# Kernel optimization log

Hardware: AMD Instinct MI355X
Metric: run time of the kernel (lower is better)

Reference implementation:

```python
import jax, jax.numpy as jnp
import numpy as np

NUM_USERS = 200000
NUM_ITEMS = 100000
N = NUM_USERS + NUM_ITEMS
EMB_DIM = 64
NUM_LAYERS = 3
NNZ = 4000000


def setup_inputs() -> dict:
    key = jax.random.key(0)
    k1, k2, k3, k4, k5 = jax.random.split(key, 5)
    # xavier_uniform: bound = sqrt(6/(fan_in+fan_out))
    bound = float(np.sqrt(6.0 / (NUM_USERS + EMB_DIM)))
    user_emb = jax.random.uniform(k1, (NUM_USERS, EMB_DIM), jnp.float32, -bound, bound)
    bound_i = float(np.sqrt(6.0 / (NUM_ITEMS + EMB_DIM)))
    item_emb = jax.random.uniform(k2, (NUM_ITEMS, EMB_DIM), jnp.float32, -bound_i, bound_i)
    rows = jax.random.randint(k3, (NNZ,), 0, N, dtype=jnp.int32)
    cols = jax.random.randint(k4, (NNZ,), 0, N, dtype=jnp.int32)
    vals = jax.random.uniform(k5, (NNZ,), jnp.float32)
    return {"user_emb": user_emb, "item_emb": item_emb,
            "rows": rows, "cols": cols, "vals": vals}


def _spmm(rows, cols, vals, x):
    # sparse (N,N) @ dense (N,D) via gather + segment-sum scatter
    gathered = vals[:, None] * x[cols]          # [nnz, D]
    return jax.ops.segment_sum(gathered, rows, num_segments=N)


def reference(user_emb, item_emb, rows, cols, vals):
    emb = jnp.concatenate([user_emb, item_emb], axis=0)  # [N, D]
    acc = emb  # running sum fuses the layer-mean (avoids stacking all layers)
    for _ in range(NUM_LAYERS):
        emb = _spmm(rows, cols, vals, emb)
        acc = acc + emb
    final = acc / (NUM_LAYERS + 1)
    return final[:NUM_USERS], final[NUM_USERS:]
```

## Files before the change

kernel.cpp:

```cpp
#include <hip/hip_runtime.h>


#define NUSERS 200000
#define NITEMS 100000
#define NNODES 300000
#define DIM 64
#define NNZ_CNT 4000000

#define SCAN_CHUNK 1024
#define NCHUNKS ((NNODES + SCAN_CHUNK - 1) / SCAN_CHUNK)
#define CNT_PAD (NCHUNKS * SCAN_CHUNK)

#define BSHIFT 10
#define BROWS  (1 << BSHIFT)
#define NB     ((NNODES + BROWS - 1) >> BSHIFT)
#define EPB    8192


__device__ __forceinline__ unsigned short f32_to_bf16(float f) {
    unsigned u = __float_as_uint(f);
    u += 0x7FFFu + ((u >> 16) & 1u);
    return (unsigned short)(u >> 16);
}
__device__ __forceinline__ float bf16_to_f32(unsigned short h) {
    return __uint_as_float(((unsigned)h) << 16);
}


__global__ void k_hist(const int* __restrict__ rows, int* __restrict__ cnt) {
    int e = blockIdx.x * blockDim.x + threadIdx.x;
    if (e >= NNZ_CNT) return;
    atomicAdd(&cnt[rows[e]], 1);
}

__global__ void k_partial(const int* __restrict__ cnt, int* __restrict__ partial) {
    int t = threadIdx.x;
    int base = blockIdx.x * SCAN_CHUNK;
    int4 c = ((const int4*)(cnt + base))[t];
    int tsum = c.x + c.y + c.z + c.w;
    __shared__ int lds[256];
    lds[t] = tsum; __syncthreads();
    for (int d = 128; d > 0; d >>= 1) {
        if (t < d) lds[t] += lds[t + d];
        __syncthreads();
    }
    if (t == 0) partial[blockIdx.x] = lds[0];
}

__global__ void k_scanpartial(const int* __restrict__ partial, int* __restrict__ partoff) {
    int t = threadIdx.x;
    int v = (t < NCHUNKS) ? partial[t] : 0;
    __shared__ int lds[512];
    lds[t] = v; __syncthreads();
    for (int d = 1; d < 512; d <<= 1) {
        int cur = lds[t];
        int add = (t >= d) ? lds[t - d] : 0;
        __syncthreads();
        lds[t] = cur + add;
        __syncthreads();
    }
    if (t < NCHUNKS) partoff[t] = lds[t] - v;
}

__global__ void k_scan3(const int* __restrict__ cnt, const int* __restrict__ partoff,
                        int* __restrict__ rowptr) {
    int t = threadIdx.x, b = blockIdx.x;
    int base = b * SCAN_CHUNK;
    int4 c = ((const int4*)(cnt + base))[t];
    int tsum = c.x + c.y + c.z + c.w;
    __shared__ int lds[256];
    lds[t] = tsum; __syncthreads();
    for (int d = 1; d < 256; d <<= 1) {
        int cur = lds[t];
        int add = (t >= d) ? lds[t - d] : 0;
        __syncthreads();
        lds[t] = cur + add;
        __syncthreads();
    }
    int excl = lds[t] - tsum;
    int off = partoff[b] + excl;
    int idx = base + t * 4;
    rowptr[idx + 0] = off;
    rowptr[idx + 1] = off + c.x;
    rowptr[idx + 2] = off + c.x + c.y;
    rowptr[idx + 3] = off + c.x + c.y + c.z;
}

__global__ void k_initcur(const int* __restrict__ rowptr, int* __restrict__ gcursor) {
    int t = blockIdx.x * blockDim.x + threadIdx.x;
    if (t >= NB) return;
    int r = t << BSHIFT;
    if (r > NNODES) r = NNODES;
    gcursor[t] = rowptr[r];
}


__global__ void __launch_bounds__(256) k_bucketA(
        const int* __restrict__ rows, const int* __restrict__ cols,
        const float* __restrict__ vals, int* __restrict__ gcursor,
        int2* __restrict__ staged) {
    __shared__ int hist[NB];
    __shared__ int lbase[NB];
    __shared__ int lcur[NB];
    int t = threadIdx.x;
    int e0 = blockIdx.x * EPB;
    for (int i = t; i < NB; i += 256) { hist[i] = 0; lcur[i] = 0; }
    __syncthreads();
    for (int k = 0; k < EPB / 256; ++k) {
        int e = e0 + k * 256 + t;
        if (e < NNZ_CNT) atomicAdd(&hist[rows[e] >> BSHIFT], 1);
    }
    __syncthreads();
    for (int i = t; i < NB; i += 256) {
        int h = hist[i];
        lbase[i] = h ? atomicAdd(&gcursor[i], h) : 0;
    }
    __syncthreads();
    for (int k = 0; k < EPB / 256; ++k) {
        int e = e0 + k * 256 + t;
        if (e >= NNZ_CNT) continue;
        int r = rows[e];
        int b = r >> BSHIFT;
        int p = lbase[b] + atomicAdd(&lcur[b], 1);
        int2 rec;
        rec.x = ((r & (BROWS - 1)) << 19) | cols[e];
        rec.y = __float_as_int(vals[e]);
        staged[p] = rec;
    }
}


__global__ void __launch_bounds__(1024) k_bucketB(
        const int* __restrict__ rowptr, const int2* __restrict__ staged,
        int2* __restrict__ packed) {
    __shared__ int cur[BROWS];
    int b = blockIdx.x;
    int t = threadIdx.x;
    int r0 = b << BSHIFT;
    int r1 = min(r0 + BROWS, NNODES);
    int nrows = r1 - r0;
    for (int i = t; i < nrows; i += 1024) cur[i] = rowptr[r0 + i];
    __syncthreads();
    int start = rowptr[r0];
    int end   = rowptr[r1];
    for (int idx = start + t; idx < end; idx += 1024) {
        int2 rec = staged[idx];
        int rel = ((unsigned)rec.x) >> 19;
        int col = rec.x & 0x7FFFF;
        int pos = atomicAdd(&cur[rel], 1);
        int2 out; out.x = col; out.y = rec.y;
        packed[pos] = out;
    }
}


__global__ void k_init0(const float* __restrict__ ue, const float* __restrict__ ie,
                        unsigned short* __restrict__ xb0, float* __restrict__ acc) {
    int i = blockIdx.x * blockDim.x + threadIdx.x;
    const int total = NNODES * DIM / 4;
    if (i >= total) return;
    const int userEnd = NUSERS * DIM / 4;
    float4 v = (i < userEnd) ? ((const float4*)ue)[i]
                             : ((const float4*)ie)[i - userEnd];
    ((float4*)acc)[i] = v;
    ushort4 h;
    h.x = f32_to_bf16(v.x); h.y = f32_to_bf16(v.y);
    h.z = f32_to_bf16(v.z); h.w = f32_to_bf16(v.w);
    ((ushort4*)xb0)[i] = h;
}


template <int FINAL>
__global__ void __launch_bounds__(256) k_spmm_csr(
                           const int* __restrict__ rowptr, const int2* __restrict__ packed,
                           const unsigned short* __restrict__ xin,
                           unsigned short* __restrict__ y, float* __restrict__ acc) {
    int row  = blockIdx.x * (blockDim.x >> 6) + (threadIdx.x >> 6);
    int lane = threadIdx.x & 63;
    if (row >= NNODES) return;
    int start = __builtin_amdgcn_readfirstlane(rowptr[row]);
    int end   = __builtin_amdgcn_readfirstlane(rowptr[row + 1]);
    const unsigned short* __restrict__ xl = xin + lane;
    float s0 = 0.f, s1 = 0.f, s2 = 0.f, s3 = 0.f;
    int idx = start;
    for (; idx + 4 <= end; idx += 4) {
        int2 e0 = packed[idx + 0];
        int2 e1 = packed[idx + 1];
        int2 e2 = packed[idx + 2];
        int2 e3 = packed[idx + 3];
        float g0 = bf16_to_f32(xl[(size_t)e0.x << 6]);
        float g1 = bf16_to_f32(xl[(size_t)e1.x << 6]);
        float g2 = bf16_to_f32(xl[(size_t)e2.x << 6]);
        float g3 = bf16_to_f32(xl[(size_t)e3.x << 6]);
        s0 += __int_as_float(e0.y) * g0;
        s1 += __int_as_float(e1.y) * g1;
        s2 += __int_as_float(e2.y) * g2;
        s3 += __int_as_float(e3.y) * g3;
    }
    for (; idx < end; ++idx) {
        int2 e = packed[idx];
        s0 += __int_as_float(e.y) * bf16_to_f32(xl[(size_t)e.x << 6]);
    }
    float s = (s0 + s1) + (s2 + s3);
    size_t o = ((size_t)row << 6) + lane;
    if (FINAL) {
        acc[o] = (acc[o] + s) * 0.25f;
    } else {
        y[o] = f32_to_bf16(s);
        acc[o] += s;
    }
}


extern "C" void kernel_launch(void* const* d_in, const int* in_sizes, int n_in,
                              void* d_out, int out_size, void* d_ws, size_t ws_size,
                              hipStream_t stream) {
    const float* ue   = (const float*)d_in[0];
    const float* ie   = (const float*)d_in[1];
    const int*   rows = (const int*)d_in[2];
    const int*   cols = (const int*)d_in[3];
    const float* vals = (const float*)d_in[4];
    float* acc = (float*)d_out;

    const size_t embN = (size_t)NNODES * DIM;
    char* p = (char*)d_ws;
    unsigned short* xb0 = (unsigned short*)p;  p += embN * 2;
    unsigned short* xb1 = (unsigned short*)p;  p += embN * 2;
    unsigned short* xb2 = (unsigned short*)p;  p += embN * 2;
    int*   rowptr = (int*)p;              p += (size_t)(CNT_PAD + 16) * 4;
    int*   cnt    = (int*)p;              p += (size_t)(CNT_PAD + 16) * 4;
    int*   part   = (int*)p;              p += 512 * 4;
    int*   poff   = (int*)p;              p += 512 * 4;
    int*   gcur   = (int*)p;              p += 512 * 4;
    int2*  staged = (int2*)p;             p += (size_t)NNZ_CNT * 8;
    int2*  packed = (int2*)p;             p += (size_t)NNZ_CNT * 8;

    const int edge_blocks = (NNZ_CNT + 255) / 256;
    const int row_blocks  = (NNODES + 3) / 4;
    const int bucketA_blocks = (NNZ_CNT + EPB - 1) / EPB;
    const int vec_blocks = (NNODES * DIM / 4 + 255) / 256;

    hipMemsetAsync(cnt, 0, (size_t)(CNT_PAD + 16) * 4, stream);
    k_hist<<<edge_blocks, 256, 0, stream>>>(rows, cnt);
    k_partial<<<NCHUNKS, 256, 0, stream>>>(cnt, part);
    k_scanpartial<<<1, 512, 0, stream>>>(part, poff);
    k_scan3<<<NCHUNKS, 256, 0, stream>>>(cnt, poff, rowptr);

    k_initcur<<<2, 256, 0, stream>>>(rowptr, gcur);
    k_bucketA<<<bucketA_blocks, 256, 0, stream>>>(rows, cols, vals, gcur, staged);
    k_bucketB<<<NB, 1024, 0, stream>>>(rowptr, staged, packed);

    k_init0<<<vec_blocks, 256, 0, stream>>>(ue, ie, xb0, acc);

    k_spmm_csr<0><<<row_blocks, 256, 0, stream>>>(rowptr, packed, xb0, xb1, acc);
    k_spmm_csr<0><<<row_blocks, 256, 0, stream>>>(rowptr, packed, xb1, xb2, acc);
    k_spmm_csr<1><<<row_blocks, 256, 0, stream>>>(rowptr, packed, xb2, (unsigned short*)nullptr, acc);
}
```

Measured before the change: 869.3 us.

## Build CSR via bucket-level histogram and in-block row scan; prefetch SpMM edges

Replaces the per-row global atomic histogram and three-kernel scan with a per-bucket histogram that uses shared-memory atomics, a single-block bucket scan, and a per-bucket row count and scan inside k_bucketB that writes rowptr directly. This removes 4M contended global atomics and several small kernel launches from the CSR build. The SpMM kernel also switches to an 8-wide loop that software-prefetches the next 8 packed edges, with masked tail handling, to hide edge-load latency behind the gathers. The costs are an extra pass over staged records in bucketB, and padded edge loads and gathers for short rows.

```diff
diff --git a/kernel.cpp b/kernel.cpp
--- a/kernel.cpp
+++ b/kernel.cpp
@@ -7,10 +7,6 @@
 #define DIM 64
 #define NNZ_CNT 4000000
 
-#define SCAN_CHUNK 1024
-#define NCHUNKS ((NNODES + SCAN_CHUNK - 1) / SCAN_CHUNK)
-#define CNT_PAD (NCHUNKS * SCAN_CHUNK)
-
 #define BSHIFT 10
 #define BROWS  (1 << BSHIFT)
 #define NB     ((NNODES + BROWS - 1) >> BSHIFT)
@@ -27,29 +23,28 @@
 }
 
 
-__global__ void k_hist(const int* __restrict__ rows, int* __restrict__ cnt) {
-    int e = blockIdx.x * blockDim.x + threadIdx.x;
-    if (e >= NNZ_CNT) return;
-    atomicAdd(&cnt[rows[e]], 1);
-}
-
-__global__ void k_partial(const int* __restrict__ cnt, int* __restrict__ partial) {
-    int t = threadIdx.x;
-    int base = blockIdx.x * SCAN_CHUNK;
-    int4 c = ((const int4*)(cnt + base))[t];
-    int tsum = c.x + c.y + c.z + c.w;
-    __shared__ int lds[256];
-    lds[t] = tsum; __syncthreads();
-    for (int d = 128; d > 0; d >>= 1) {
-        if (t < d) lds[t] += lds[t + d];
-        __syncthreads();
-    }
-    if (t == 0) partial[blockIdx.x] = lds[0];
-}
-
-__global__ void k_scanpartial(const int* __restrict__ partial, int* __restrict__ partoff) {
-    int t = threadIdx.x;
-    int v = (t < NCHUNKS) ? partial[t] : 0;
+__global__ void __launch_bounds__(256) k_bhist(const int* __restrict__ rows,
+                                               int* __restrict__ bcnt) {
+    __shared__ int hist[NB];
+    int t = threadIdx.x;
+    int e0 = blockIdx.x * EPB;
+    for (int i = t; i < NB; i += 256) hist[i] = 0;
+    __syncthreads();
+    for (int k = 0; k < EPB / 256; ++k) {
+        int e = e0 + k * 256 + t;
+        if (e < NNZ_CNT) atomicAdd(&hist[rows[e] >> BSHIFT], 1);
+    }
+    __syncthreads();
+    for (int i = t; i < NB; i += 256) {
+        int h = hist[i];
+        if (h) atomicAdd(&bcnt[i], h);
+    }
+}
+
+__global__ void k_bscan(const int* __restrict__ bcnt, int* __restrict__ bbase,
+                        int* __restrict__ gcur) {
+    int t = threadIdx.x;
+    int v = (t < NB) ? bcnt[t] : 0;
     __shared__ int lds[512];
     lds[t] = v; __syncthreads();
     for (int d = 1; d < 512; d <<= 1) {
@@ -59,39 +54,12 @@
         lds[t] = cur + add;
         __syncthreads();
     }
-    if (t < NCHUNKS) partoff[t] = lds[t] - v;
-}
-
-__global__ void k_scan3(const int* __restrict__ cnt, const int* __restrict__ partoff,
-                        int* __restrict__ rowptr) {
-    int t = threadIdx.x, b = blockIdx.x;
-    int base = b * SCAN_CHUNK;
-    int4 c = ((const int4*)(cnt + base))[t];
-    int tsum = c.x + c.y + c.z + c.w;
-    __shared__ int lds[256];
-    lds[t] = tsum; __syncthreads();
-    for (int d = 1; d < 256; d <<= 1) {
-        int cur = lds[t];
-        int add = (t >= d) ? lds[t - d] : 0;
-        __syncthreads();
-        lds[t] = cur + add;
-        __syncthreads();
-    }
-    int excl = lds[t] - tsum;
-    int off = partoff[b] + excl;
-    int idx = base + t * 4;
-    rowptr[idx + 0] = off;
-    rowptr[idx + 1] = off + c.x;
-    rowptr[idx + 2] = off + c.x + c.y;
-    rowptr[idx + 3] = off + c.x + c.y + c.z;
-}
-
-__global__ void k_initcur(const int* __restrict__ rowptr, int* __restrict__ gcursor) {
-    int t = blockIdx.x * blockDim.x + threadIdx.x;
-    if (t >= NB) return;
-    int r = t << BSHIFT;
-    if (r > NNODES) r = NNODES;
-    gcursor[t] = rowptr[r];
+    if (t < NB) {
+        int e = lds[t] - v;
+        bbase[t] = e;
+        gcur[t]  = e;
+    }
+    if (t == 511) bbase[NB] = lds[511];
 }
 
 
@@ -131,18 +99,36 @@
 
 
 __global__ void __launch_bounds__(1024) k_bucketB(
-        const int* __restrict__ rowptr, const int2* __restrict__ staged,
-        int2* __restrict__ packed) {
+        const int* __restrict__ bbase, const int2* __restrict__ staged,
+        int2* __restrict__ packed, int* __restrict__ rowptr) {
+    __shared__ int rcnt[BROWS];
     __shared__ int cur[BROWS];
     int b = blockIdx.x;
     int t = threadIdx.x;
     int r0 = b << BSHIFT;
     int r1 = min(r0 + BROWS, NNODES);
     int nrows = r1 - r0;
-    for (int i = t; i < nrows; i += 1024) cur[i] = rowptr[r0 + i];
-    __syncthreads();
-    int start = rowptr[r0];
-    int end   = rowptr[r1];
+    rcnt[t] = 0;
+    __syncthreads();
+    int start = bbase[b];
+    int end   = bbase[b + 1];
+    const int* sx = (const int*)staged;
+    for (int idx = start + t; idx < end; idx += 1024)
+        atomicAdd(&rcnt[((unsigned)sx[idx << 1]) >> 19], 1);
+    __syncthreads();
+    int v = rcnt[t];
+    for (int d = 1; d < 1024; d <<= 1) {
+        int c = rcnt[t];
+        int a = (t >= d) ? rcnt[t - d] : 0;
+        __syncthreads();
+        rcnt[t] = c + a;
+        __syncthreads();
+    }
+    int excl = rcnt[t] - v;
+    cur[t] = start + excl;
+    if (t < nrows) rowptr[r0 + t] = start + excl;
+    if (b == NB - 1 && t == 0) rowptr[NNODES] = end;
+    __syncthreads();
     for (int idx = start + t; idx < end; idx += 1024) {
         int2 rec = staged[idx];
         int rel = ((unsigned)rec.x) >> 19;
@@ -181,33 +167,45 @@
     int start = __builtin_amdgcn_readfirstlane(rowptr[row]);
     int end   = __builtin_amdgcn_readfirstlane(rowptr[row + 1]);
     const unsigned short* __restrict__ xl = xin + lane;
-    float s0 = 0.f, s1 = 0.f, s2 = 0.f, s3 = 0.f;
-    int idx = start;
-    for (; idx + 4 <= end; idx += 4) {
-        int2 e0 = packed[idx + 0];
-        int2 e1 = packed[idx + 1];
-        int2 e2 = packed[idx + 2];
-        int2 e3 = packed[idx + 3];
-        float g0 = bf16_to_f32(xl[(size_t)e0.x << 6]);
-        float g1 = bf16_to_f32(xl[(size_t)e1.x << 6]);
-        float g2 = bf16_to_f32(xl[(size_t)e2.x << 6]);
-        float g3 = bf16_to_f32(xl[(size_t)e3.x << 6]);
-        s0 += __int_as_float(e0.y) * g0;
-        s1 += __int_as_float(e1.y) * g1;
-        s2 += __int_as_float(e2.y) * g2;
-        s3 += __int_as_float(e3.y) * g3;
-    }
-    for (; idx < end; ++idx) {
-        int2 e = packed[idx];
-        s0 += __int_as_float(e.y) * bf16_to_f32(xl[(size_t)e.x << 6]);
-    }
-    float s = (s0 + s1) + (s2 + s3);
+    float s[8];
+    #pragma unroll
+    for (int j = 0; j < 8; ++j) s[j] = 0.f;
+
+    if (start < end) {
+        int2 e[8];
+        #pragma unroll
+        for (int j = 0; j < 8; ++j) {
+            int k = start + j;
+            e[j] = packed[(k < end) ? k : start];
+        }
+        for (int base = start; base < end; base += 8) {
+            int nb = base + 8;
+            int2 en[8];
+            #pragma unroll
+            for (int j = 0; j < 8; ++j) {
+                int k = nb + j;
+                en[j] = packed[(k < end) ? k : start];
+            }
+            #pragma unroll
+            for (int j = 0; j < 8; ++j) {
+                bool m = (base + j) < end;
+                float g = bf16_to_f32(xl[(size_t)e[j].x << 6]);
+                float v = m ? __int_as_float(e[j].y) : 0.0f;
+                s[j] += v * g;
+            }
+            #pragma unroll
+            for (int j = 0; j < 8; ++j) e[j] = en[j];
+        }
+    }
+    float t0 = (s[0] + s[1]) + (s[2] + s[3]);
+    float t1 = (s[4] + s[5]) + (s[6] + s[7]);
+    float ssum = t0 + t1;
     size_t o = ((size_t)row << 6) + lane;
     if (FINAL) {
-        acc[o] = (acc[o] + s) * 0.25f;
+        acc[o] = (acc[o] + ssum) * 0.25f;
     } else {
-        y[o] = f32_to_bf16(s);
-        acc[o] += s;
+        y[o] = f32_to_bf16(ssum);
+        acc[o] += ssum;
     }
 }
 
@@ -227,28 +225,23 @@
     unsigned short* xb0 = (unsigned short*)p;  p += embN * 2;
     unsigned short* xb1 = (unsigned short*)p;  p += embN * 2;
     unsigned short* xb2 = (unsigned short*)p;  p += embN * 2;
-    int*   rowptr = (int*)p;              p += (size_t)(CNT_PAD + 16) * 4;
-    int*   cnt    = (int*)p;              p += (size_t)(CNT_PAD + 16) * 4;
-    int*   part   = (int*)p;              p += 512 * 4;
-    int*   poff   = (int*)p;              p += 512 * 4;
+    int*   rowptr = (int*)p;              p += (size_t)(NNODES + 16) * 4;
+    int*   bcnt   = (int*)p;              p += 512 * 4;
+    int*   bbase  = (int*)p;              p += 512 * 4;
     int*   gcur   = (int*)p;              p += 512 * 4;
     int2*  staged = (int2*)p;             p += (size_t)NNZ_CNT * 8;
     int2*  packed = (int2*)p;             p += (size_t)NNZ_CNT * 8;
 
-    const int edge_blocks = (NNZ_CNT + 255) / 256;
     const int row_blocks  = (NNODES + 3) / 4;
-    const int bucketA_blocks = (NNZ_CNT + EPB - 1) / EPB;
+    const int edge_hblocks = (NNZ_CNT + EPB - 1) / EPB;
     const int vec_blocks = (NNODES * DIM / 4 + 255) / 256;
 
-    hipMemsetAsync(cnt, 0, (size_t)(CNT_PAD + 16) * 4, stream);
-    k_hist<<<edge_blocks, 256, 0, stream>>>(rows, cnt);
-    k_partial<<<NCHUNKS, 256, 0, stream>>>(cnt, part);
-    k_scanpartial<<<1, 512, 0, stream>>>(part, poff);
-    k_scan3<<<NCHUNKS, 256, 0, stream>>>(cnt, poff, rowptr);
-
-    k_initcur<<<2, 256, 0, stream>>>(rowptr, gcur);
-    k_bucketA<<<bucketA_blocks, 256, 0, stream>>>(rows, cols, vals, gcur, staged);
-    k_bucketB<<<NB, 1024, 0, stream>>>(rowptr, staged, packed);
+    hipMemsetAsync(bcnt, 0, 512 * 4, stream);
+    k_bhist<<<edge_hblocks, 256, 0, stream>>>(rows, bcnt);
+    k_bscan<<<1, 512, 0, stream>>>(bcnt, bbase, gcur);
+
+    k_bucketA<<<edge_hblocks, 256, 0, stream>>>(rows, cols, vals, gcur, staged);
+    k_bucketB<<<NB, 1024, 0, stream>>>(bbase, staged, packed, rowptr);
 
     k_init0<<<vec_blocks, 256, 0, stream>>>(ue, ie, xb0, acc);
 
```

Measured after the change: 816.6 us. 6.1% less time.
